# Kernel optimization log

Hardware: AMD Instinct MI355X
Metric: run time of the kernel (lower is better)

Reference implementation:

```python
import jax, jax.numpy as jnp
import numpy as np
import math

B, T, D, H, V = 32, 512, 256, 4, 5000
NL = 6          # transformer layers
DUR_CAP = 8     # cap per-token duration so output length is static under jit
T_OUT = 2048    # fixed regulated length (avg duration ~1-2 with small init)


def _layernorm(x, g, b, eps=1e-5):
    m = jnp.mean(x, axis=-1, keepdims=True)
    v = jnp.var(x, axis=-1, keepdims=True)
    return (x - m) * jax.lax.rsqrt(v + eps) * g + b


def _conv1d(x, w, b):
    # x [B,C,T], w [O,I,K] -> [B,O,T], 'same' padding as in torch
    pad = (w.shape[-1] - 1) // 2
    y = jax.lax.conv_general_dilated(x, w, (1,), [(pad, pad)],
                                     dimension_numbers=('NCH', 'OIH', 'NCH'))
    return y + b[None, :, None]


def _pos_encoding(t, d):
    pos = jnp.arange(t, dtype=jnp.float32)[:, None]
    div = jnp.exp(jnp.arange(0, d, 2, dtype=jnp.float32) * (-math.log(10000.0) / d))
    ang = pos * div  # [t, d/2]
    return jnp.stack([jnp.sin(ang), jnp.cos(ang)], axis=-1).reshape(t, d)


def setup_inputs():
    key = jax.random.key(0)
    ks = iter(jax.random.split(key, 64))
    def nrm(shape, s=0.02):
        return jax.random.normal(next(ks), shape, dtype=jnp.float32) * s
    return {
        'text': jax.random.randint(next(ks), (B, T), 0, V, dtype=jnp.int32),
        'emotion': jax.random.normal(next(ks), (B, 1), dtype=jnp.float32),
        'emb': nrm((V, D), 1.0),
        'Wqkv': nrm((NL, D, 3 * D)), 'bqkv': jnp.zeros((NL, 3 * D)),
        'Wo': nrm((NL, D, D)), 'bo': jnp.zeros((NL, D)),
        'W1': nrm((NL, D, 4 * D)), 'b1': jnp.zeros((NL, 4 * D)),
        'W2': nrm((NL, 4 * D, D)), 'b2': jnp.zeros((NL, D)),
        'ln1g': jnp.ones((NL, D)), 'ln1b': jnp.zeros((NL, D)),
        'ln2g': jnp.ones((NL, D)), 'ln2b': jnp.zeros((NL, D)),
        'We1': nrm((1, 64), 0.1), 'be1': jnp.zeros((64,)),
        'We2': nrm((64, D), 0.1), 'be2': jnp.zeros((D,)),
        'dp_w1': nrm((D, D, 3)), 'dp_b1': jnp.zeros((D,)),
        'dp_g1': jnp.ones((D,)), 'dp_bt1': jnp.zeros((D,)),
        'dp_m1': jnp.zeros((D,)), 'dp_v1': jnp.ones((D,)),
        'dp_w2': nrm((D, D, 3)), 'dp_b2': jnp.zeros((D,)),
        'dp_g2': jnp.ones((D,)), 'dp_bt2': jnp.zeros((D,)),
        'dp_m2': jnp.zeros((D,)), 'dp_v2': jnp.ones((D,)),
        'dp_wo': nrm((1, D, 1)), 'dp_bo': jnp.zeros((1,)),
        'dec_w1': nrm((256, D, 5)), 'dec_b1': jnp.zeros((256,)),
        'dec_w2': nrm((128, 256, 5)), 'dec_b2': jnp.zeros((128,)),
        'dec_w3': nrm((1, 128, 5)), 'dec_b3': jnp.zeros((1,)),
    }


def reference(text, emotion, emb, Wqkv, bqkv, Wo, bo, W1, b1, W2, b2,
              ln1g, ln1b, ln2g, ln2b, We1, be1, We2, be2,
              dp_w1, dp_b1, dp_g1, dp_bt1, dp_m1, dp_v1,
              dp_w2, dp_b2, dp_g2, dp_bt2, dp_m2, dp_v2, dp_wo, dp_bo,
              dec_w1, dec_b1, dec_w2, dec_b2, dec_w3, dec_b3):
    dh = D // H
    scale = 1.0 / math.sqrt(dh)
    x = emb[text] + _pos_encoding(T, D)[None]  # [B,T,D]
    # post-norm TransformerEncoder (torch default), relu FFN, eval mode
    for i in range(NL):
        qkv = x @ Wqkv[i] + bqkv[i]
        q, k, v = jnp.split(qkv, 3, axis=-1)
        q = q.reshape(B, T, H, dh); k = k.reshape(B, T, H, dh); v = v.reshape(B, T, H, dh)
        att = jax.nn.softmax(jnp.einsum('bthd,bshd->bhts', q, k) * scale, axis=-1)
        o = jnp.einsum('bhts,bshd->bthd', att, v).reshape(B, T, D) @ Wo[i] + bo[i]
        x = _layernorm(x + o, ln1g[i], ln1b[i])
        ff = jax.nn.relu(x @ W1[i] + b1[i]) @ W2[i] + b2[i]
        x = _layernorm(x + ff, ln2g[i], ln2b[i])
    # EmotionFusion (assumed additive MLP projection, output_dim = 256)
    e = jax.nn.relu(emotion @ We1 + be1) @ We2 + be2  # [B,256]
    fused = x + e[:, None, :]                          # [B,T,D]
    # DurationPredictor (eval: BN with running stats, dropout off)
    def bn(y, g, bt, m, vv):
        return g[None, :, None] * (y - m[None, :, None]) * jax.lax.rsqrt(vv + 1e-5)[None, :, None] + bt[None, :, None]
    h = fused.transpose(0, 2, 1)  # [B,D,T]
    h = bn(jax.nn.relu(_conv1d(h, dp_w1, dp_b1)), dp_g1, dp_bt1, dp_m1, dp_v1)
    h = bn(jax.nn.relu(_conv1d(h, dp_w2, dp_b2)), dp_g2, dp_bt2, dp_m2, dp_v2)
    log_dur = _conv1d(h, dp_wo, dp_bo)[:, 0, :]  # [B,T]
    dur = jnp.clip(jnp.round(jnp.exp(log_dur)), 1, DUR_CAP).astype(jnp.int32)
    dur = jax.lax.stop_gradient(dur)
    # LengthRegulator: repeat token i dur[i] times, zero-pad to T_OUT
    def regulate(xb, db):
        total = jnp.sum(db)
        pad = jnp.maximum(T_OUT - total, 0)
        xe = jnp.concatenate([xb, jnp.zeros((1, D), xb.dtype)], axis=0)
        de = jnp.concatenate([db, pad[None]], axis=0)
        return jnp.repeat(xe, de, axis=0, total_repeat_length=T_OUT)
    reg = jax.vmap(regulate)(fused, dur)  # [B,T_OUT,D]
    # decoder conv stack
    y = reg.transpose(0, 2, 1)
    y = jax.nn.relu(_conv1d(y, dec_w1, dec_b1))
    y = jax.nn.relu(_conv1d(y, dec_w2, dec_b2))
    wav = _conv1d(y, dec_w3, dec_b3)[:, 0, :]  # [B,T_OUT]
    return wav
```

## Files before the change

### kernel.cpp

```cpp
#include <hip/hip_runtime.h>
#include <math.h>

#define NB 32
#define NT 512
#define ND 256
#define NH 4
#define NLAYER 6
#define TOUT 2048

typedef __attribute__((ext_vector_type(8))) short bf16x8;
typedef __attribute__((ext_vector_type(4))) float f32x4;
typedef __attribute__((ext_vector_type(16))) float f32x16;

static __device__ __forceinline__ unsigned short f2b(float f) {
    union { float f; unsigned int u; } x; x.f = f;
    unsigned int u = x.u;
    return (unsigned short)((u + 0x7FFFu + ((u >> 16) & 1u)) >> 16);
}
static __device__ __forceinline__ float b2f(unsigned short s) {
    union { unsigned int u; float f; } x; x.u = ((unsigned int)s) << 16;
    return x.f;
}

#define SW(r) (((r) >> 1) & 3)

#define OFF_X    0ull
#define OFF_FFH  4194304ull
#define OFF_WBT  12582912ull
#define OFF_CWT  14942208ull
#define OFF_QKV  20971520ull
#define OFF_ATTN 33554432ull
#define OFF_PROJ 37748736ull
#define OFF_INT  41951232ull

__global__ __launch_bounds__(256) void embed_kernel(const int* __restrict__ text,
                                                    const float* __restrict__ emb,
                                                    float* __restrict__ x)
{
    const int row = blockIdx.x;
    const int d = threadIdx.x;
    const int t = row & (NT - 1);
    const int id = text[row];
    const int j2 = (d >> 1) * 2;
    const float c = -9.210340371976184f / 256.0f;
    float freq = expf((float)j2 * c);
    float ang = (float)t * freq;
    float pe = (d & 1) ? cosf(ang) : sinf(ang);
    x[(size_t)row * ND + d] = emb[(size_t)id * ND + d] + pe;
}

__global__ __launch_bounds__(256) void wqall_kernel(const float* __restrict__ Wqkv,
                                                    const float* __restrict__ Wo,
                                                    const float* __restrict__ W1,
                                                    const float* __restrict__ W2,
                                                    unsigned short* __restrict__ Wbt)
{
    __shared__ float tile[32][33];
    const int tt = blockIdx.x, layer = blockIdx.y;
    const float* src; int K, N, n0, k0, inLS; size_t outSeg;
    if (tt < 192)      { src = Wqkv; K = 256;  N = 768;  n0 = (tt % 24) * 32; k0 = (tt / 24) * 32; inLS = 196608; outSeg = 0; }
    else if (tt < 256) { int t2 = tt - 192; src = Wo; K = 256; N = 256;  n0 = (t2 & 7) * 32;  k0 = (t2 >> 3) * 32; inLS = 65536;  outSeg = 196608; }
    else if (tt < 512) { int t3 = tt - 256; src = W1; K = 256; N = 1024; n0 = (t3 & 31) * 32; k0 = (t3 >> 5) * 32; inLS = 262144; outSeg = 262144; }
    else               { int t4 = tt - 512; src = W2; K = 1024; N = 256; n0 = (t4 & 7) * 32;  k0 = (t4 >> 3) * 32; inLS = 262144; outSeg = 524288; }
    const float* Wl = src + (size_t)layer * inLS;
    unsigned short* ol = Wbt + (size_t)layer * 786432 + outSeg;
    const int tx = threadIdx.x & 31, ty = threadIdx.x >> 5;
#pragma unroll
    for (int j = 0; j < 4; ++j)
        tile[ty + j * 8][tx] = Wl[(size_t)(k0 + ty + j * 8) * N + n0 + tx];
    __syncthreads();
#pragma unroll
    for (int j = 0; j < 4; ++j)
        ol[(size_t)(n0 + ty + j * 8) * K + k0 + tx] = f2b(tile[tx][ty + j * 8]);
}

__global__ __launch_bounds__(256) void wtransball_kernel(const float* __restrict__ dp_w1,
                                                         const float* __restrict__ dp_w2,
                                                         const float* __restrict__ dec_w1,
                                                         const float* __restrict__ dec_w2,
                                                         unsigned short* __restrict__ cw)
{
    int gid = blockIdx.x * 256 + threadIdx.x;
    if (gid >= 884736) return;
    const float* src; int CIN = 256, COUT, KS, idx;
    if (gid < 196608)      { src = dp_w1;  COUT = 256; KS = 3; idx = gid; }
    else if (gid < 393216) { src = dp_w2;  COUT = 256; KS = 3; idx = gid - 196608; }
    else if (gid < 720896) { src = dec_w1; COUT = 256; KS = 5; idx = gid - 393216; }
    else                   { src = dec_w2; COUT = 128; KS = 5; idx = gid - 720896; }
    int c = idx % CIN;
    int r = idx / CIN;
    int o = r % COUT;
    int k = r / COUT;
    cw[gid] = f2b(src[(o * CIN + c) * KS + k]);
}

template<int NTILE, bool RELU, bool ABF16, bool CBF16, bool VOUT>
__global__ __launch_bounds__(256) void gemmbf_kernel(const void* __restrict__ A_,
                                                     const unsigned short* __restrict__ Bt,
                                                     const float* __restrict__ bias,
                                                     void* __restrict__ C_,
                                                     unsigned short* __restrict__ vt,
                                                     int M, int N, int K)
{
    constexpr int MT = (NTILE == 128) ? 2 : 1;
    __shared__ __align__(16) unsigned short Asb[128 * 32];
    __shared__ __align__(16) unsigned short Bsb[NTILE * 32];
    const int tid = threadIdx.x;
    const int lane = tid & 63, wave = tid >> 6;
    const int ln = lane & 31, hi = lane >> 5;
    const int row0 = blockIdx.y * 128, col0 = blockIdx.x * NTILE;
    const int mOff = (NTILE == 128) ? (wave >> 1) * 64 : wave * 32;
    const int nOff = (NTILE == 128) ? (wave & 1) * 64 : 0;
    const float* Af = (const float*)A_;
    const unsigned short* Ab = (const unsigned short*)A_;
    float* Cf = (float*)C_;
    unsigned short* Cb = (unsigned short*)C_;
    f32x16 acc[MT][2] = {};

    for (int k0 = 0; k0 < K; k0 += 32) {
#pragma unroll
        for (int it = 0; it < 2; ++it) {
            int u = it * 256 + tid;
            int m = u >> 2, blk = u & 3;
            unsigned short s8[8];
            if (ABF16) {
                *(uint4*)s8 = *(const uint4*)&Ab[(size_t)(row0 + m) * K + k0 + blk * 8];
            } else {
                float4 v0 = *(const float4*)&Af[(size_t)(row0 + m) * K + k0 + blk * 8];
                float4 v1 = *(const float4*)&Af[(size_t)(row0 + m) * K + k0 + blk * 8 + 4];
                s8[0] = f2b(v0.x); s8[1] = f2b(v0.y); s8[2] = f2b(v0.z); s8[3] = f2b(v0.w);
                s8[4] = f2b(v1.x); s8[5] = f2b(v1.y); s8[6] = f2b(v1.z); s8[7] = f2b(v1.w);
            }
            *(uint4*)&Asb[m * 32 + ((blk ^ SW(m)) << 3)] = *(uint4*)s8;
        }
#pragma unroll
        for (int it = 0; it < NTILE / 64; ++it) {
            int u = it * 256 + tid;
            int n = u >> 2, blk = u & 3;
            *(uint4*)&Bsb[n * 32 + ((blk ^ SW(n)) << 3)] =
                *(const uint4*)&Bt[(size_t)(col0 + n) * K + k0 + blk * 8];
        }
        __syncthreads();
#pragma unroll
        for (int kh = 0; kh < 2; ++kh) {
            const int kb = kh * 2 + hi;
            bf16x8 af[MT], bfr[2];
#pragma unroll
            for (int mt = 0; mt < MT; ++mt) {
                int r = mOff + mt * 32 + ln;
                af[mt] = *(const bf16x8*)&Asb[r * 32 + ((kb ^ SW(r)) << 3)];
            }
#pragma unroll
            for (int nt = 0; nt < 2; ++nt) {
                int r = nOff + nt * 32 + ln;
                bfr[nt] = *(const bf16x8*)&Bsb[r * 32 + ((kb ^ SW(r)) << 3)];
            }
#pragma unroll
            for (int mt = 0; mt < MT; ++mt)
#pragma unroll
                for (int nt = 0; nt < 2; ++nt)
                    acc[mt][nt] = __builtin_amdgcn_mfma_f32_32x32x16_bf16(
                        af[mt], bfr[nt], acc[mt][nt], 0, 0, 0);
        }
        __syncthreads();
    }
#pragma unroll
    for (int mt = 0; mt < MT; ++mt)
#pragma unroll
        for (int nt = 0; nt < 2; ++nt) {
            int col = col0 + nOff + nt * 32 + ln;
            float bi = bias[col];
#pragma unroll
            for (int g = 0; g < 4; ++g) {
                unsigned short s4[4];
#pragma unroll
                for (int r4 = 0; r4 < 4; ++r4) {
                    int row = row0 + mOff + mt * 32 + hi * 4 + g * 8 + r4;
                    float v = acc[mt][nt][g * 4 + r4] + bi;
                    if (RELU) v = fmaxf(v, 0.f);
                    if (CBF16) { s4[r4] = f2b(v); Cb[(size_t)row * N + col] = s4[r4]; }
                    else       Cf[(size_t)row * N + col] = v;
                }
                if (VOUT && col >= 512) {
                    int rowg = row0 + mOff + mt * 32 + hi * 4 + g * 8;
                    int b = rowg >> 9, t = rowg & (NT - 1);
                    int hh = (col - 512) >> 6, dd = (col - 512) & 63;
                    *(uint2*)&vt[((size_t)(b * NH + hh) * 64 + dd) * NT + t] = *(uint2*)s4;
                }
            }
        }
}

__global__ __launch_bounds__(256, 2) void attn3_kernel(const unsigned short* __restrict__ qkv,
                                                       const unsigned short* __restrict__ vt,
                                                       unsigned short* __restrict__ out)
{
    __shared__ __align__(16) unsigned short sP[4][32 * 64];
    const int tid = threadIdx.x;
    const int lane = tid & 63, wave = tid >> 6;
    const int ln = lane & 31, hi = lane >> 5;
    const int h = blockIdx.y, b = blockIdx.z;
    const int q0 = blockIdx.x * 128 + wave * 32;
    const size_t base = (size_t)b * NT * 768;
    const int qoff = h * 64;
    const unsigned short* vbh = vt + (size_t)(b * NH + h) * 64 * NT;

    bf16x8 qf[4];
#pragma unroll
    for (int s = 0; s < 4; ++s)
        qf[s] = *(const bf16x8*)&qkv[base + (size_t)(q0 + ln) * 768 + qoff + s * 16 + hi * 8];

    float mrow[16], lrow[16];
#pragma unroll
    for (int i = 0; i < 16; ++i) { mrow[i] = -1e30f; lrow[i] = 0.f; }
    f32x16 oacc[2] = {};
    const float sc = 0.18033688011112042f;
    const int i0 = (ln & 3) | (((ln >> 3) & 3) << 2);
    const bool own = (((ln >> 2) & 1) == hi);
    unsigned short* Pw = &sP[wave][0];

    for (int ch = 0; ch < 8; ++ch) {
        const int s0 = ch * 64;
        f32x16 sacc[2] = {};
#pragma unroll
        for (int ct = 0; ct < 2; ++ct)
#pragma unroll
            for (int s = 0; s < 4; ++s) {
                bf16x8 kf = *(const bf16x8*)&qkv[base + (size_t)(s0 + ct * 32 + ln) * 768
                                                 + 256 + qoff + s * 16 + hi * 8];
                sacc[ct] = __builtin_amdgcn_mfma_f32_32x32x16_bf16(qf[s], kf, sacc[ct], 0, 0, 0);
            }
        float alpha[16];
#pragma unroll
        for (int i = 0; i < 16; ++i) {
            float s20 = sacc[0][i] * sc, s21 = sacc[1][i] * sc;
            float mx = fmaxf(s20, s21);
#pragma unroll
            for (int o = 1; o < 32; o <<= 1) mx = fmaxf(mx, __shfl_xor(mx, o));
            float mn = fmaxf(mrow[i], mx);
            alpha[i] = exp2f(mrow[i] - mn);
            mrow[i] = mn;
            float p0 = exp2f(s20 - mn);
            float p1 = exp2f(s21 - mn);
            sacc[0][i] = p0; sacc[1][i] = p1;
            float rs = p0 + p1;
#pragma unroll
            for (int o = 1; o < 32; o <<= 1) rs += __shfl_xor(rs, o);
            lrow[i] = lrow[i] * alpha[i] + rs;
        }
#pragma unroll
        for (int ct = 0; ct < 2; ++ct) {
            int kb = ct * 4 + (ln >> 3), k7 = ln & 7;
#pragma unroll
            for (int i = 0; i < 16; ++i) {
                int q = (i & 3) + 8 * (i >> 2) + 4 * hi;
                Pw[q * 64 + (((kb ^ (q & 7)) << 3) | k7)] = f2b(sacc[ct][i]);
            }
        }
        __syncthreads();
        {
            float av = alpha[i0];
            float ao = __shfl_xor(av, 32);
            float aq = own ? av : ao;
#pragma unroll
            for (int ct = 0; ct < 2; ++ct)
#pragma unroll
                for (int i = 0; i < 16; ++i)
                    oacc[ct][i] *= aq;
        }
#pragma unroll
        for (int s = 0; s < 4; ++s) {
            bf16x8 pf = *(const bf16x8*)&Pw[ln * 64 + (((s * 2 + hi) ^ (ln & 7)) << 3)];
#pragma unroll
            for (int ct = 0; ct < 2; ++ct) {
                bf16x8 vf = *(const bf16x8*)&vbh[(size_t)(ct * 32 + ln) * NT + s0 + s * 16 + hi * 8];
                oacc[ct] = __builtin_amdgcn_mfma_f32_32x32x16_bf16(vf, pf, oacc[ct], 0, 0, 0);
            }
        }
        __syncthreads();
    }
    float lv = lrow[i0];
    float lo = __shfl_xor(lv, 32);
    float linv = 1.0f / (own ? lv : lo);
    const int q = q0 + ln;
#pragma unroll
    for (int ct = 0; ct < 2; ++ct)
#pragma unroll
        for (int i = 0; i < 16; ++i) {
            int d = ct * 32 + (i & 3) + 8 * (i >> 2) + 4 * hi;
            out[(size_t)(b * NT + q) * ND + qoff + d] = f2b(oacc[ct][i] * linv);
        }
}

__global__ __launch_bounds__(256) void add_ln_kernel(float* __restrict__ x,
                                                     const float* __restrict__ y,
                                                     const float* __restrict__ g,
                                                     const float* __restrict__ bta)
{
    const int w = threadIdx.x >> 6, lane = threadIdx.x & 63;
    const size_t row = (size_t)blockIdx.x * 4 + w;
    const int c4 = lane * 4;
    float4 xv = *(const float4*)&x[row * ND + c4];
    float4 yv = *(const float4*)&y[row * ND + c4];
    float4 v = make_float4(xv.x + yv.x, xv.y + yv.y, xv.z + yv.z, xv.w + yv.w);
    float s = v.x + v.y + v.z + v.w;
#pragma unroll
    for (int o = 1; o < 64; o <<= 1) s += __shfl_xor(s, o);
    float m = s * (1.0f / 256.0f);
    float4 dv = make_float4(v.x - m, v.y - m, v.z - m, v.w - m);
    float s2 = dv.x * dv.x + dv.y * dv.y + dv.z * dv.z + dv.w * dv.w;
#pragma unroll
    for (int o = 1; o < 64; o <<= 1) s2 += __shfl_xor(s2, o);
    float r = 1.0f / sqrtf(s2 * (1.0f / 256.0f) + 1e-5f);
    float4 gv = *(const float4*)&g[c4];
    float4 bv = *(const float4*)&bta[c4];
    float4 o4 = make_float4(dv.x * r * gv.x + bv.x, dv.y * r * gv.y + bv.y,
                            dv.z * r * gv.z + bv.z, dv.w * r * gv.w + bv.w);
    *(float4*)&x[row * ND + c4] = o4;
}

__global__ __launch_bounds__(256) void fuse_kernel(const float* __restrict__ emo,
                                                   const float* __restrict__ We1,
                                                   const float* __restrict__ be1,
                                                   const float* __restrict__ We2,
                                                   const float* __restrict__ be2,
                                                   float* __restrict__ x)
{
    const int row = blockIdx.x;
    const int d = threadIdx.x;
    const float em = emo[row >> 9];
    float acc = be2[d];
    for (int j = 0; j < 64; ++j) {
        float h = fmaxf(em * We1[j] + be1[j], 0.0f);
        acc = fmaf(h, We2[j * ND + d], acc);
    }
    x[(size_t)row * ND + d] += acc;
}

template<int CIN, int KS, bool IN_BF16, bool OUT_BF16, bool BN>
__global__ __launch_bounds__(256) void convk_kernel(const void* __restrict__ in_,
                                                    const unsigned short* __restrict__ wtb,
                                                    const float* __restrict__ bias,
                                                    const float* __restrict__ bng,
                                                    const float* __restrict__ bnb,
                                                    const float* __restrict__ bnm,
                                                    const float* __restrict__ bnv,
                                                    void* __restrict__ out_,
                                                    int T, int COUT)
{
    constexpr int PAD = (KS - 1) / 2;
    constexpr int TEXT = 128 + KS - 1;
    __shared__ __align__(16) unsigned short Asb[TEXT * 32];
    __shared__ __align__(16) unsigned short Bsb[KS * 64 * 32];
    const int tid = threadIdx.x;
    const int lane = tid & 63, wave = tid >> 6;
    const int ln = lane & 31, hi = lane >> 5;
    const int b = blockIdx.z;
    const int t0 = blockIdx.x * 128;
    const int o0 = blockIdx.y * 64;
    const int mOff = wave * 32;
    const float* inf = (const float*)in_;
    const unsigned short* inb = (const unsigned short*)in_;
    float* outf = (float*)out_;
    unsigned short* outb = (unsigned short*)out_;
    f32x16 acc[2] = {};

    for (int cc = 0; cc < CIN; cc += 32) {
        for (int u = tid; u < TEXT * 4; u += 256) {
            int t = u >> 2, blk = u & 3;
            int tg = t0 - PAD + t;
            unsigned short s8[8] = {0, 0, 0, 0, 0, 0, 0, 0};
            if (tg >= 0 && tg < T) {
                if (IN_BF16) {
                    *(uint4*)s8 = *(const uint4*)&inb[((size_t)(b * T) + tg) * CIN + cc + blk * 8];
                } else {
                    float4 v0 = *(const float4*)&inf[((size_t)(b * T) + tg) * CIN + cc + blk * 8];
                    float4 v1 = *(const float4*)&inf[((size_t)(b * T) + tg) * CIN + cc + blk * 8 + 4];
                    s8[0] = f2b(v0.x); s8[1] = f2b(v0.y); s8[2] = f2b(v0.z); s8[3] = f2b(v0.w);
                    s8[4] = f2b(v1.x); s8[5] = f2b(v1.y); s8[6] = f2b(v1.z); s8[7] = f2b(v1.w);
                }
            }
            *(uint4*)&Asb[t * 32 + ((blk ^ SW(t)) << 3)] = *(uint4*)s8;
        }
        for (int u = tid; u < KS * 256; u += 256) {
            int row = u >> 2, blk = u & 3;
            int k = row >> 6, o = row & 63;
            *(uint4*)&Bsb[row * 32 + ((blk ^ SW(row)) << 3)] =
                *(const uint4*)&wtb[((size_t)k * COUT + o0 + o) * CIN + cc + blk * 8];
        }
        __syncthreads();
#pragma unroll
        for (int kh = 0; kh < 2; ++kh) {
            const int kb = kh * 2 + hi;
            bf16x8 af[KS];
#pragma unroll
            for (int tap = 0; tap < KS; ++tap) {
                int r = mOff + ln + tap;
                af[tap] = *(const bf16x8*)&Asb[r * 32 + ((kb ^ SW(r)) << 3)];
            }
#pragma unroll
            for (int nt = 0; nt < 2; ++nt) {
#pragma unroll
                for (int tap = 0; tap < KS; ++tap) {
                    int rb = tap * 64 + nt * 32 + ln;
                    bf16x8 bfr = *(const bf16x8*)&Bsb[rb * 32 + ((kb ^ SW(rb)) << 3)];
                    acc[nt] = __builtin_amdgcn_mfma_f32_32x32x16_bf16(af[tap], bfr, acc[nt], 0, 0, 0);
                }
            }
        }
        __syncthreads();
    }
#pragma unroll
    for (int nt = 0; nt < 2; ++nt) {
        int col = o0 + nt * 32 + ln;
        float bi = bias[col];
        float scv = 1.f, shv = 0.f;
        if (BN) {
            scv = bng[col] / sqrtf(bnv[col] + 1e-5f);
            shv = bnb[col] - bnm[col] * scv;
        }
#pragma unroll
        for (int g = 0; g < 4; ++g)
#pragma unroll
            for (int r4 = 0; r4 < 4; ++r4) {
                int row = t0 + mOff + hi * 4 + g * 8 + r4;
                float v = fmaxf(acc[nt][g * 4 + r4] + bi, 0.f);
                if (BN) v = v * scv + shv;
                if (OUT_BF16) outb[((size_t)(b * T) + row) * COUT + col] = f2b(v);
                else          outf[((size_t)(b * T) + row) * COUT + col] = v;
            }
    }
}

__global__ __launch_bounds__(256) void reg_kernel(const float* __restrict__ x,
                                                  const int* __restrict__ tok,
                                                  unsigned short* __restrict__ reg)
{
    const int wave = threadIdx.x >> 6, lane = threadIdx.x & 63;
    const int row = blockIdx.x * 4 + wave;
    const int tk = tok[row];
    const int b = row >> 11;
    const int c4 = lane * 4;
    unsigned short s4[4] = {0, 0, 0, 0};
    if (tk >= 0) {
        float4 v = *(const float4*)&x[((size_t)(b * NT) + tk) * ND + c4];
        s4[0] = f2b(v.x); s4[1] = f2b(v.y); s4[2] = f2b(v.z); s4[3] = f2b(v.w);
    }
    *(uint2*)&reg[(size_t)row * ND + c4] = *(uint2*)s4;
}

__global__ __launch_bounds__(256) void dur_kernel(const float* __restrict__ h2,
                                                  const float* __restrict__ wo,
                                                  const float* __restrict__ bo,
                                                  int* __restrict__ dur)
{
    const int wave = threadIdx.x >> 6, lane = threadIdx.x & 63;
    const int row = blockIdx.x * 4 + wave;
    const int c4 = lane * 4;
    float4 h = *(const float4*)&h2[(size_t)row * ND + c4];
    float4 w4 = *(const float4*)&wo[c4];
    float s = h.x * w4.x + h.y * w4.y + h.z * w4.z + h.w * w4.w;
#pragma unroll
    for (int o = 1; o < 64; o <<= 1) s += __shfl_xor(s, o);
    if (lane == 0) {
        float d = rintf(expf(s + bo[0]));
        d = fminf(fmaxf(d, 1.0f), 8.0f);
        dur[row] = (int)d;
    }
}

__global__ __launch_bounds__(256) void scantok_kernel(const int* __restrict__ dur,
                                                      int* __restrict__ tok)
{
    __shared__ int st[NT];
    __shared__ int tot;
    const int b = blockIdx.x, tid = threadIdx.x;
    if (tid == 0) {
        int a = 0;
        for (int t = 0; t < NT; ++t) { st[t] = a; a += dur[b * NT + t]; }
        tot = a;
    }
    __syncthreads();
    for (int p = tid; p < TOUT; p += 256) {
        int res = -1;
        if (p < tot) {
            int lo = 0, hi = NT - 1;
            while (lo < hi) {
                int mid = (lo + hi + 1) >> 1;
                if (st[mid] <= p) lo = mid; else hi = mid - 1;
            }
            res = lo;
        }
        tok[b * TOUT + p] = res;
    }
}

__global__ __launch_bounds__(256) void conv3_kernel(const unsigned short* __restrict__ in,
                                                    const float* __restrict__ w,
                                                    const float* __restrict__ bias,
                                                    float* __restrict__ out)
{
    const int wave = threadIdx.x >> 6, lane = threadIdx.x & 63;
    const int gid = blockIdx.x * 4 + wave;
    const int b = gid >> 11, t = gid & (TOUT - 1);
    const int c = lane * 2;
    float w0[5], w1[5];
#pragma unroll
    for (int k = 0; k < 5; ++k) { w0[k] = w[c * 5 + k]; w1[k] = w[(c + 1) * 5 + k]; }
    float acc = 0.f;
#pragma unroll
    for (int k = 0; k < 5; ++k) {
        int t2 = t + k - 2;
        if (t2 < 0 || t2 >= TOUT) continue;
        unsigned int u = *(const unsigned int*)&in[((size_t)(b * TOUT) + t2) * 128 + c];
        acc = fmaf(b2f((unsigned short)(u & 0xFFFF)), w0[k], acc);
        acc = fmaf(b2f((unsigned short)(u >> 16)), w1[k], acc);
    }
#pragma unroll
    for (int o = 1; o < 64; o <<= 1) acc += __shfl_xor(acc, o);
    if (lane == 0) out[gid] = acc + bias[0];
}

extern "C" void kernel_launch(void* const* d_in, const int* in_sizes, int n_in,
                              void* d_out, int out_size, void* d_ws, size_t ws_size,
                              hipStream_t stream)
{
    const int*   text    = (const int*)d_in[0];
    const float* emotion = (const float*)d_in[1];
    const float* emb     = (const float*)d_in[2];
    const float* Wqkv    = (const float*)d_in[3];
    const float* bqkv    = (const float*)d_in[4];
    const float* Wo      = (const float*)d_in[5];
    const float* bo      = (const float*)d_in[6];
    const float* W1      = (const float*)d_in[7];
    const float* b1      = (const float*)d_in[8];
    const float* W2      = (const float*)d_in[9];
    const float* b2      = (const float*)d_in[10];
    const float* ln1g    = (const float*)d_in[11];
    const float* ln1b    = (const float*)d_in[12];
    const float* ln2g    = (const float*)d_in[13];
    const float* ln2b    = (const float*)d_in[14];
    const float* We1     = (const float*)d_in[15];
    const float* be1     = (const float*)d_in[16];
    const float* We2     = (const float*)d_in[17];
    const float* be2     = (const float*)d_in[18];
    const float* dp_w1   = (const float*)d_in[19];
    const float* dp_b1   = (const float*)d_in[20];
    const float* dp_g1   = (const float*)d_in[21];
    const float* dp_bt1  = (const float*)d_in[22];
    const float* dp_m1   = (const float*)d_in[23];
    const float* dp_v1   = (const float*)d_in[24];
    const float* dp_w2   = (const float*)d_in[25];
    const float* dp_b2   = (const float*)d_in[26];
    const float* dp_g2   = (const float*)d_in[27];
    const float* dp_bt2  = (const float*)d_in[28];
    const float* dp_m2   = (const float*)d_in[29];
    const float* dp_v2   = (const float*)d_in[30];
    const float* dp_wo   = (const float*)d_in[31];
    const float* dp_bo   = (const float*)d_in[32];
    const float* dec_w3  = (const float*)d_in[37];
    const float* dec_b1  = (const float*)d_in[34];
    const float* dec_b2  = (const float*)d_in[36];
    const float* dec_b3  = (const float*)d_in[38];

    float* ws   = (float*)d_ws;
    float* x    = ws + OFF_X;
    unsigned short* ffhB = (unsigned short*)(ws + OFF_FFH);
    unsigned short* Wbt  = (unsigned short*)(ws + OFF_WBT);
    unsigned short* cw   = (unsigned short*)(ws + OFF_CWT);
    unsigned short* wtbdp1 = cw;
    unsigned short* wtbdp2 = cw + 196608;
    unsigned short* wtb1   = cw + 393216;
    unsigned short* wtb2   = cw + 720896;
    unsigned short* qkvB = (unsigned short*)(ws + OFF_QKV);
    unsigned short* vtb  = qkvB + 12582912;
    unsigned short* regB = qkvB;
    float* attb = ws + OFF_ATTN;
    float* prjb = ws + OFF_PROJ;
    unsigned short* attbB = (unsigned short*)attb;
    unsigned short* h1b  = (unsigned short*)attb;
    unsigned short* d1b  = ffhB;
    unsigned short* d2b  = (unsigned short*)attb;
    int*   ip     = (int*)(ws + OFF_INT);
    int*   durb   = ip;
    int*   tokb   = ip + 16384;

    const int M = NB * NT;

    embed_kernel<<<M, 256, 0, stream>>>(text, emb, x);
    wqall_kernel<<<dim3(768, 6), 256, 0, stream>>>(Wqkv, Wo, W1, W2, Wbt);
    wtransball_kernel<<<3456, 256, 0, stream>>>(dp_w1, dp_w2,
                                                (const float*)d_in[33], (const float*)d_in[35], cw);

    for (int l = 0; l < NLAYER; ++l) {
        const unsigned short* WQ  = Wbt + (size_t)l * 786432;
        const unsigned short* WO  = WQ + 196608;
        const unsigned short* WF1 = WQ + 262144;
        const unsigned short* WF2 = WQ + 524288;
        gemmbf_kernel<128, false, false, true, true><<<dim3(6, 128), 256, 0, stream>>>(
            x, WQ, bqkv + l * 768, qkvB, vtb, M, 768, 256);
        attn3_kernel<<<dim3(NT / 128, NH, NB), 256, 0, stream>>>(qkvB, vtb, attbB);
        gemmbf_kernel<64, false, true, false, false><<<dim3(4, 128), 256, 0, stream>>>(
            attbB, WO, bo + l * 256, prjb, nullptr, M, 256, 256);
        add_ln_kernel<<<M / 4, 256, 0, stream>>>(x, prjb, ln1g + l * ND, ln1b + l * ND);
        gemmbf_kernel<128, true, false, true, false><<<dim3(8, 128), 256, 0, stream>>>(
            x, WF1, b1 + l * 1024, ffhB, nullptr, M, 1024, 256);
        gemmbf_kernel<64, false, true, false, false><<<dim3(4, 128), 256, 0, stream>>>(
            ffhB, WF2, b2 + l * 256, prjb, nullptr, M, 256, 1024);
        add_ln_kernel<<<M / 4, 256, 0, stream>>>(x, prjb, ln2g + l * ND, ln2b + l * ND);
    }

    fuse_kernel<<<M, 256, 0, stream>>>(emotion, We1, be1, We2, be2, x);

    convk_kernel<256, 3, false, true, true><<<dim3(4, 4, NB), 256, 0, stream>>>(
        x, wtbdp1, dp_b1, dp_g1, dp_bt1, dp_m1, dp_v1, h1b, NT, 256);
    convk_kernel<256, 3, true, false, true><<<dim3(4, 4, NB), 256, 0, stream>>>(
        h1b, wtbdp2, dp_b2, dp_g2, dp_bt2, dp_m2, dp_v2, prjb, NT, 256);
    dur_kernel<<<M / 4, 256, 0, stream>>>(prjb, dp_wo, dp_bo, durb);
    scantok_kernel<<<NB, 256, 0, stream>>>(durb, tokb);

    reg_kernel<<<NB * TOUT / 4, 256, 0, stream>>>(x, tokb, regB);
    convk_kernel<256, 5, true, true, false><<<dim3(TOUT / 128, 4, NB), 256, 0, stream>>>(
        regB, wtb1, dec_b1, nullptr, nullptr, nullptr, nullptr, d1b, TOUT, 256);
    convk_kernel<256, 5, true, true, false><<<dim3(TOUT / 128, 2, NB), 256, 0, stream>>>(
        d1b, wtb2, dec_b2, nullptr, nullptr, nullptr, nullptr, d2b, TOUT, 128);
    conv3_kernel<<<NB * TOUT / 4, 256, 0, stream>>>(d2b, dec_w3, dec_b3, (float*)d_out);
}
```

Baseline: 1.498 ms.

## Fuse output-projection GEMMs with residual add and LayerNorm; enlarge conv time tiles

Adds a GEMM kernel that computes a full 256-column row block, adds bias and the residual, and applies LayerNorm in the epilogue through a cross-wave shared-memory reduction. It replaces the Wo and W2 GEMMs plus their separate add_ln passes, which removes the fp32 intermediate write and re-read and two launches per layer. The conv kernel tile also grows from 128 to 256 time steps, with each wave computing two M sub-tiles so B fragments and weights are reused more. In exchange the fused GEMM launches only 256 blocks, which may underfill the GPU, and variance now comes from E[x^2]-m^2, which is slightly less numerically robust.

Result: no change. 1.473 ms (-1.7%).

```diff
diff --git a/kernel.cpp b/kernel.cpp
--- a/kernel.cpp
+++ b/kernel.cpp
@@ -191,6 +191,108 @@
         }
 }
 
+__global__ __launch_bounds__(256) void gemmln_kernel(const unsigned short* __restrict__ A,
+                                                     const unsigned short* __restrict__ Bt,
+                                                     const float* __restrict__ bias,
+                                                     const float* __restrict__ lng,
+                                                     const float* __restrict__ lnb,
+                                                     float* __restrict__ x,
+                                                     int K)
+{
+    __shared__ __align__(16) unsigned short Asb[64 * 32];
+    __shared__ __align__(16) unsigned short Bsb[256 * 32];
+    __shared__ float sred[64][2][2];
+    const int tid = threadIdx.x;
+    const int lane = tid & 63, wave = tid >> 6;
+    const int ln = lane & 31, hi = lane >> 5;
+    const int row0 = blockIdx.x * 64;
+    const int mOff = (wave >> 1) * 32;
+    const int colbase = (wave & 1) * 128;
+    f32x16 acc[4] = {};
+
+    for (int k0 = 0; k0 < K; k0 += 32) {
+        {
+            int m = tid >> 2, blk = tid & 3;
+            *(uint4*)&Asb[m * 32 + ((blk ^ SW(m)) << 3)] =
+                *(const uint4*)&A[(size_t)(row0 + m) * K + k0 + blk * 8];
+        }
+#pragma unroll
+        for (int it = 0; it < 4; ++it) {
+            int u = it * 256 + tid;
+            int n = u >> 2, blk = u & 3;
+            *(uint4*)&Bsb[n * 32 + ((blk ^ SW(n)) << 3)] =
+                *(const uint4*)&Bt[(size_t)n * K + k0 + blk * 8];
+        }
+        __syncthreads();
+#pragma unroll
+        for (int kh = 0; kh < 2; ++kh) {
+            const int kb = kh * 2 + hi;
+            int r = mOff + ln;
+            bf16x8 af = *(const bf16x8*)&Asb[r * 32 + ((kb ^ SW(r)) << 3)];
+#pragma unroll
+            for (int nt = 0; nt < 4; ++nt) {
+                int rb = colbase + nt * 32 + ln;
+                bf16x8 bfr = *(const bf16x8*)&Bsb[rb * 32 + ((kb ^ SW(rb)) << 3)];
+                acc[nt] = __builtin_amdgcn_mfma_f32_32x32x16_bf16(af, bfr, acc[nt], 0, 0, 0);
+            }
+        }
+        __syncthreads();
+    }
+
+    float bi[4], gv[4], bv[4];
+#pragma unroll
+    for (int nt = 0; nt < 4; ++nt) {
+        int col = colbase + nt * 32 + ln;
+        bi[nt] = bias[col]; gv[nt] = lng[col]; bv[nt] = lnb[col];
+    }
+#pragma unroll
+    for (int g = 0; g < 4; ++g)
+#pragma unroll
+        for (int r4 = 0; r4 < 4; ++r4) {
+            int rl = mOff + hi * 4 + g * 8 + r4;
+            size_t base = (size_t)(row0 + rl) * ND + colbase + ln;
+#pragma unroll
+            for (int nt = 0; nt < 4; ++nt)
+                acc[nt][g * 4 + r4] += bi[nt] + x[base + nt * 32];
+        }
+#pragma unroll
+    for (int g = 0; g < 4; ++g)
+#pragma unroll
+        for (int r4 = 0; r4 < 4; ++r4) {
+            int i = g * 4 + r4;
+            float ps = acc[0][i] + acc[1][i] + acc[2][i] + acc[3][i];
+            float ps2 = acc[0][i] * acc[0][i] + acc[1][i] * acc[1][i]
+                      + acc[2][i] * acc[2][i] + acc[3][i] * acc[3][i];
+#pragma unroll
+            for (int o = 1; o < 32; o <<= 1) {
+                ps += __shfl_xor(ps, o);
+                ps2 += __shfl_xor(ps2, o);
+            }
+            if (ln == 0) {
+                int rl = mOff + hi * 4 + g * 8 + r4;
+                sred[rl][wave & 1][0] = ps;
+                sred[rl][wave & 1][1] = ps2;
+            }
+        }
+    __syncthreads();
+#pragma unroll
+    for (int g = 0; g < 4; ++g)
+#pragma unroll
+        for (int r4 = 0; r4 < 4; ++r4) {
+            int i = g * 4 + r4;
+            int rl = mOff + hi * 4 + g * 8 + r4;
+            float s = sred[rl][0][0] + sred[rl][1][0];
+            float s2 = sred[rl][0][1] + sred[rl][1][1];
+            float m = s * (1.0f / 256.0f);
+            float var = fmaxf(s2 * (1.0f / 256.0f) - m * m, 0.0f);
+            float rinv = 1.0f / sqrtf(var + 1e-5f);
+            size_t base = (size_t)(row0 + rl) * ND + colbase + ln;
+#pragma unroll
+            for (int nt = 0; nt < 4; ++nt)
+                x[base + nt * 32] = (acc[nt][i] - m) * rinv * gv[nt] + bv[nt];
+        }
+}
+
 __global__ __launch_bounds__(256, 2) void attn3_kernel(const unsigned short* __restrict__ qkv,
                                                        const unsigned short* __restrict__ vt,
                                                        unsigned short* __restrict__ out)
@@ -290,33 +392,6 @@
             int d = ct * 32 + (i & 3) + 8 * (i >> 2) + 4 * hi;
             out[(size_t)(b * NT + q) * ND + qoff + d] = f2b(oacc[ct][i] * linv);
         }
-}
-
-__global__ __launch_bounds__(256) void add_ln_kernel(float* __restrict__ x,
-                                                     const float* __restrict__ y,
-                                                     const float* __restrict__ g,
-                                                     const float* __restrict__ bta)
-{
-    const int w = threadIdx.x >> 6, lane = threadIdx.x & 63;
-    const size_t row = (size_t)blockIdx.x * 4 + w;
-    const int c4 = lane * 4;
-    float4 xv = *(const float4*)&x[row * ND + c4];
-    float4 yv = *(const float4*)&y[row * ND + c4];
-    float4 v = make_float4(xv.x + yv.x, xv.y + yv.y, xv.z + yv.z, xv.w + yv.w);
-    float s = v.x + v.y + v.z + v.w;
-#pragma unroll
-    for (int o = 1; o < 64; o <<= 1) s += __shfl_xor(s, o);
-    float m = s * (1.0f / 256.0f);
-    float4 dv = make_float4(v.x - m, v.y - m, v.z - m, v.w - m);
-    float s2 = dv.x * dv.x + dv.y * dv.y + dv.z * dv.z + dv.w * dv.w;
-#pragma unroll
-    for (int o = 1; o < 64; o <<= 1) s2 += __shfl_xor(s2, o);
-    float r = 1.0f / sqrtf(s2 * (1.0f / 256.0f) + 1e-5f);
-    float4 gv = *(const float4*)&g[c4];
-    float4 bv = *(const float4*)&bta[c4];
-    float4 o4 = make_float4(dv.x * r * gv.x + bv.x, dv.y * r * gv.y + bv.y,
-                            dv.z * r * gv.z + bv.z, dv.w * r * gv.w + bv.w);
-    *(float4*)&x[row * ND + c4] = o4;
 }
 
 __global__ __launch_bounds__(256) void fuse_kernel(const float* __restrict__ emo,
@@ -349,21 +424,21 @@
                                                     int T, int COUT)
 {
     constexpr int PAD = (KS - 1) / 2;
-    constexpr int TEXT = 128 + KS - 1;
+    constexpr int TEXT = 256 + KS - 1;
     __shared__ __align__(16) unsigned short Asb[TEXT * 32];
     __shared__ __align__(16) unsigned short Bsb[KS * 64 * 32];
     const int tid = threadIdx.x;
     const int lane = tid & 63, wave = tid >> 6;
     const int ln = lane & 31, hi = lane >> 5;
     const int b = blockIdx.z;
-    const int t0 = blockIdx.x * 128;
+    const int t0 = blockIdx.x * 256;
     const int o0 = blockIdx.y * 64;
-    const int mOff = wave * 32;
+    const int mOff = wave * 64;
     const float* inf = (const float*)in_;
     const unsigned short* inb = (const unsigned short*)in_;
     float* outf = (float*)out_;
     unsigned short* outb = (unsigned short*)out_;
-    f32x16 acc[2] = {};
+    f32x16 acc[2][2] = {};
 
     for (int cc = 0; cc < CIN; cc += 32) {
         for (int u = tid; u < TEXT * 4; u += 256) {
@@ -392,19 +467,22 @@
 #pragma unroll
         for (int kh = 0; kh < 2; ++kh) {
             const int kb = kh * 2 + hi;
-            bf16x8 af[KS];
 #pragma unroll
             for (int tap = 0; tap < KS; ++tap) {
-                int r = mOff + ln + tap;
-                af[tap] = *(const bf16x8*)&Asb[r * 32 + ((kb ^ SW(r)) << 3)];
-            }
-#pragma unroll
-            for (int nt = 0; nt < 2; ++nt) {
-#pragma unroll
-                for (int tap = 0; tap < KS; ++tap) {
+                bf16x8 af[2];
+#pragma unroll
+                for (int mt = 0; mt < 2; ++mt) {
+                    int r = mOff + mt * 32 + ln + tap;
+                    af[mt] = *(const bf16x8*)&Asb[r * 32 + ((kb ^ SW(r)) << 3)];
+                }
+#pragma unroll
+                for (int nt = 0; nt < 2; ++nt) {
                     int rb = tap * 64 + nt * 32 + ln;
                     bf16x8 bfr = *(const bf16x8*)&Bsb[rb * 32 + ((kb ^ SW(rb)) << 3)];
-                    acc[nt] = __builtin_amdgcn_mfma_f32_32x32x16_bf16(af[tap], bfr, acc[nt], 0, 0, 0);
+#pragma unroll
+                    for (int mt = 0; mt < 2; ++mt)
+                        acc[mt][nt] = __builtin_amdgcn_mfma_f32_32x32x16_bf16(
+                            af[mt], bfr, acc[mt][nt], 0, 0, 0);
                 }
             }
         }
@@ -420,15 +498,17 @@
             shv = bnb[col] - bnm[col] * scv;
         }
 #pragma unroll
-        for (int g = 0; g < 4; ++g)
-#pragma unroll
-            for (int r4 = 0; r4 < 4; ++r4) {
-                int row = t0 + mOff + hi * 4 + g * 8 + r4;
-                float v = fmaxf(acc[nt][g * 4 + r4] + bi, 0.f);
-                if (BN) v = v * scv + shv;
-                if (OUT_BF16) outb[((size_t)(b * T) + row) * COUT + col] = f2b(v);
-                else          outf[((size_t)(b * T) + row) * COUT + col] = v;
-            }
+        for (int mt = 0; mt < 2; ++mt)
+#pragma unroll
+            for (int g = 0; g < 4; ++g)
+#pragma unroll
+                for (int r4 = 0; r4 < 4; ++r4) {
+                    int row = t0 + mOff + mt * 32 + hi * 4 + g * 8 + r4;
+                    float v = fmaxf(acc[mt][nt][g * 4 + r4] + bi, 0.f);
+                    if (BN) v = v * scv + shv;
+                    if (OUT_BF16) outb[((size_t)(b * T) + row) * COUT + col] = f2b(v);
+                    else          outf[((size_t)(b * T) + row) * COUT + col] = v;
+                }
     }
 }
 
@@ -600,29 +680,27 @@
         gemmbf_kernel<128, false, false, true, true><<<dim3(6, 128), 256, 0, stream>>>(
             x, WQ, bqkv + l * 768, qkvB, vtb, M, 768, 256);
         attn3_kernel<<<dim3(NT / 128, NH, NB), 256, 0, stream>>>(qkvB, vtb, attbB);
-        gemmbf_kernel<64, false, true, false, false><<<dim3(4, 128), 256, 0, stream>>>(
-            attbB, WO, bo + l * 256, prjb, nullptr, M, 256, 256);
-        add_ln_kernel<<<M / 4, 256, 0, stream>>>(x, prjb, ln1g + l * ND, ln1b + l * ND);
+        gemmln_kernel<<<M / 64, 256, 0, stream>>>(
+            attbB, WO, bo + l * 256, ln1g + l * ND, ln1b + l * ND, x, 256);
         gemmbf_kernel<128, true, false, true, false><<<dim3(8, 128), 256, 0, stream>>>(
             x, WF1, b1 + l * 1024, ffhB, nullptr, M, 1024, 256);
-        gemmbf_kernel<64, false, true, false, false><<<dim3(4, 128), 256, 0, stream>>>(
-            ffhB, WF2, b2 + l * 256, prjb, nullptr, M, 256, 1024);
-        add_ln_kernel<<<M / 4, 256, 0, stream>>>(x, prjb, ln2g + l * ND, ln2b + l * ND);
+        gemmln_kernel<<<M / 64, 256, 0, stream>>>(
+            ffhB, WF2, b2 + l * 256, ln2g + l * ND, ln2b + l * ND, x, 1024);
     }
 
     fuse_kernel<<<M, 256, 0, stream>>>(emotion, We1, be1, We2, be2, x);
 
-    convk_kernel<256, 3, false, true, true><<<dim3(4, 4, NB), 256, 0, stream>>>(
+    convk_kernel<256, 3, false, true, true><<<dim3(2, 4, NB), 256, 0, stream>>>(
         x, wtbdp1, dp_b1, dp_g1, dp_bt1, dp_m1, dp_v1, h1b, NT, 256);
-    convk_kernel<256, 3, true, false, true><<<dim3(4, 4, NB), 256, 0, stream>>>(
+    convk_kernel<256, 3, true, false, true><<<dim3(2, 4, NB), 256, 0, stream>>>(
         h1b, wtbdp2, dp_b2, dp_g2, dp_bt2, dp_m2, dp_v2, prjb, NT, 256);
     dur_kernel<<<M / 4, 256, 0, stream>>>(prjb, dp_wo, dp_bo, durb);
     scantok_kernel<<<NB, 256, 0, stream>>>(durb, tokb);
 
     reg_kernel<<<NB * TOUT / 4, 256, 0, stream>>>(x, tokb, regB);
-    convk_kernel<256, 5, true, true, false><<<dim3(TOUT / 128, 4, NB), 256, 0, stream>>>(
+    convk_kernel<256, 5, true, true, false><<<dim3(TOUT / 256, 4, NB), 256, 0, stream>>>(
         regB, wtb1, dec_b1, nullptr, nullptr, nullptr, nullptr, d1b, TOUT, 256);
-    convk_kernel<256, 5, true, true, false><<<dim3(TOUT / 128, 2, NB), 256, 0, stream>>>(
+    convk_kernel<256, 5, true, true, false><<<dim3(TOUT / 256, 2, NB), 256, 0, stream>>>(
         d1b, wtb2, dec_b2, nullptr, nullptr, nullptr, nullptr, d2b, TOUT, 128);
     conv3_kernel<<<NB * TOUT / 4, 256, 0, stream>>>(d2b, dec_w3, dec_b3, (float*)d_out);
 }
```
